# Performance work log

Measured on AMD Instinct MI355X. Metric: run time of the kernel, lower is better.

## Reference

```python
import jax, jax.numpy as jnp
import numpy as np

HIDDEN = 2048
N_HEADS = 16
HEAD_DIM = HIDDEN // N_HEADS
ROPE_THETA = 10000.0
BSZ, SEQ = 2, 2048
NEG_INF = -1e9


def setup_inputs() -> dict:
    key = jax.random.key(0)
    ks = jax.random.split(key, 5)
    scale = 1.0 / np.sqrt(HIDDEN)
    hidden_states = jax.random.normal(ks[0], (BSZ, SEQ, HIDDEN), dtype=jnp.float32)
    Wq = jax.random.normal(ks[1], (HIDDEN, HIDDEN), dtype=jnp.float32) * scale
    Wk = jax.random.normal(ks[2], (HIDDEN, HIDDEN), dtype=jnp.float32) * scale
    Wv = jax.random.normal(ks[3], (HIDDEN, HIDDEN), dtype=jnp.float32) * scale
    Wo = jax.random.normal(ks[4], (HIDDEN, HIDDEN), dtype=jnp.float32) * scale
    # additive causal mask, [1, 1, S, S]
    causal = jnp.triu(jnp.full((SEQ, SEQ), NEG_INF, dtype=jnp.float32), k=1)
    attention_mask = causal[None, None, :, :]
    position_ids = jnp.arange(SEQ, dtype=jnp.int32)
    return {
        "hidden_states": hidden_states,
        "Wq": Wq, "Wk": Wk, "Wv": Wv, "Wo": Wo,
        "attention_mask": attention_mask,
        "position_ids": position_ids,
    }


def _rotate_half(x):
    half = x.shape[-1] // 2
    return jnp.concatenate((-x[..., half:], x[..., :half]), axis=-1)


def _rope_tables(seq_len, position_ids):
    # inv_freq: [head_dim/2]
    inv_freq = 1.0 / (ROPE_THETA ** (jnp.arange(0, HEAD_DIM, 2, dtype=jnp.float32) / HEAD_DIM))
    t = jnp.arange(seq_len, dtype=jnp.float32)
    freqs = t[:, None] * inv_freq[None, :]              # [S, D/2]
    emb = jnp.concatenate((freqs, freqs), axis=-1)      # [S, D]
    cos = jnp.cos(emb)[position_ids]                    # [S, D]
    sin = jnp.sin(emb)[position_ids]
    return cos, sin


def reference(hidden_states, Wq, Wk, Wv, Wo, attention_mask, position_ids):
    b, s, h = hidden_states.shape
    def proj(W):
        return (hidden_states @ W.T).reshape(b, s, N_HEADS, HEAD_DIM).transpose(0, 2, 1, 3)
    q = proj(Wq)  # [B, H, S, D]
    k = proj(Wk)
    v = proj(Wv)
    cos, sin = _rope_tables(s, position_ids)            # [S, D], broadcasts over B,H
    q = q * cos + _rotate_half(q) * sin
    k = k * cos + _rotate_half(k) * sin
    scores = jnp.einsum('bhqd,bhkd->bhqk', q, k) / np.sqrt(HEAD_DIM)
    scores = scores + attention_mask
    w = jax.nn.softmax(scores, axis=-1)
    out = jnp.einsum('bhqk,bhkd->bhqd', w, v)           # [B, H, S, D]
    out = out.transpose(0, 2, 1, 3).reshape(b, s, h)
    return out @ Wo.T
```

## Files before the change

### kernel.cpp

```cpp
#include <hip/hip_runtime.h>
#include <cstdint>
#include <cstddef>

typedef __bf16 bf16;
typedef __bf16 bf16x4 __attribute__((ext_vector_type(4)));
typedef __bf16 bf16x8 __attribute__((ext_vector_type(8)));
typedef float  f32x4  __attribute__((ext_vector_type(4)));
typedef short  s16x4  __attribute__((ext_vector_type(4)));

#define HIDDEN 2048
#define NHEADS 16
#define HDIM   128
#define BSZ    2
#define SEQ    2048
#define BS     (BSZ*SEQ)
#define QKW    (2*HIDDEN)

union b4u { bf16x4 h; s16x4 s; };

__device__ __forceinline__ void async16(const bf16* g, bf16* l) {
    __builtin_amdgcn_global_load_lds(
        (const __attribute__((address_space(1))) unsigned int*)g,
        (__attribute__((address_space(3))) unsigned int*)l, 16, 0, 0);
}

#define BARX()  asm volatile("s_barrier" ::: "memory")
#define VMW(N)  asm volatile("s_waitcnt vmcnt(" #N ")" ::: "memory")

__device__ __forceinline__ float ex2(float x) {
    float r; asm("v_exp_f32 %0, %1" : "=v"(r) : "v"(x)); return r;
}

__global__ __launch_bounds__(256) void cast_all(const float* __restrict__ hs,
                                                const float* __restrict__ Wq,
                                                const float* __restrict__ Wk,
                                                const float* __restrict__ Wv,
                                                const float* __restrict__ Wo,
                                                const int* __restrict__ pos,
                                                bf16* __restrict__ hs_b,
                                                bf16* __restrict__ wqkv,
                                                bf16* __restrict__ wo_b,
                                                float2* __restrict__ tab) {
    int i = blockIdx.x * 256 + threadIdx.x;
    if (i >= 6291456) {
        int j = i - 6291456;
        int s = j >> 6, p = j & 63;
        float t = (float)pos[s];
        float inv = expf(-(float)(2 * p) * (9.2103403719761836f / 128.0f));
        float sn, cs;
        sincosf(t * inv, &sn, &cs);
        tab[j] = make_float2(cs, sn);
        return;
    }
    const float* src; bf16* dst; int off;
    if (i < 2097152) { src = hs; dst = hs_b; off = i; }
    else {
        int j = i - 2097152;
        int r = j >> 20;
        off = j & 1048575;
        if      (r == 0) { src = Wq; dst = wqkv; }
        else if (r == 1) { src = Wk; dst = wqkv + (size_t)4194304; }
        else if (r == 2) { src = Wv; dst = wqkv + (size_t)8388608; }
        else             { src = Wo; dst = wo_b; }
    }
    const float4 v = ((const float4*)src)[off];
    bf16x4 o;
    o.x = (bf16)v.x; o.y = (bf16)v.y; o.z = (bf16)v.z; o.w = (bf16)v.w;
    ((bf16x4*)dst)[off] = o;
}

__device__ __forceinline__ int qk_perm(int n) {
    int wl = n >> 6, j = n & 63;
    return ((wl >> 1) << 7) | ((j >> 5) << 6) | ((wl & 1) << 5) | (j & 31);
}

#define QKV_TILE(T, DOSTAGE, VMN) do {                                          \
    VMW(VMN);                                                                   \
    BARX();                                                                     \
    const bf16* lAr = lA0 + ((T) & 3) * 16384;                                  \
    const bf16* lBr = lB0 + ((T) & 3) * 16384;                                  \
    bf16x8 bfr[4], af[4];                                                       \
    _Pragma("unroll") for (int nf = 0; nf < 4; ++nf)                            \
        bfr[nf] = *(const bf16x8*)(lBr + nf * 512);                             \
    _Pragma("unroll") for (int mf = 0; mf < 4; ++mf)                            \
        af[mf] = *(const bf16x8*)(lAr + mf * 512);                              \
    if (DOSTAGE) {                                                              \
        bf16* dA = smem + (((T) + 3) & 3) * 16384 + w * 512;                    \
        async16(pa0 + ((T) + 3) * 32, dA);                                      \
        async16(pa1 + ((T) + 3) * 32, dA + 4096);                               \
    }                                                                           \
    __builtin_amdgcn_s_setprio(1);                                              \
    _Pragma("unroll") for (int mf = 0; mf < 4; ++mf)                            \
    _Pragma("unroll") for (int nf = 0; nf < 4; ++nf)                            \
        acc[mf][nf] = __builtin_amdgcn_mfma_f32_16x16x32_bf16(                  \
            af[mf], bfr[nf], acc[mf][nf], 0, 0, 0);                             \
    __builtin_amdgcn_s_setprio(0);                                              \
    _Pragma("unroll") for (int mf = 0; mf < 4; ++mf)                            \
        af[mf] = *(const bf16x8*)(lAr + 2048 + mf * 512);                       \
    if (DOSTAGE) {                                                              \
        bf16* dB = smem + (((T) + 3) & 3) * 16384 + 8192 + w * 512;             \
        async16(pb0 + ((T) + 3) * 32, dB);                                      \
        async16(pb1 + ((T) + 3) * 32, dB + 4096);                               \
    }                                                                           \
    __builtin_amdgcn_s_setprio(1);                                              \
    _Pragma("unroll") for (int mf = 0; mf < 4; ++mf)                            \
    _Pragma("unroll") for (int nf = 0; nf < 4; ++nf)                            \
        acc[4 + mf][nf] = __builtin_amdgcn_mfma_f32_16x16x32_bf16(              \
            af[mf], bfr[nf], acc[4 + mf][nf], 0, 0, 0);                         \
    __builtin_amdgcn_s_setprio(0);                                              \
} while (0)

__global__ __launch_bounds__(512, 2) void gemm_qk(const bf16* __restrict__ A,
                                                  const bf16* __restrict__ Bt,
                                                  const float2* __restrict__ tab,
                                                  bf16* __restrict__ qk) {
    __shared__ alignas(16) bf16 smem[65536];

    const int tid  = threadIdx.x;
    const int lane = tid & 63;
    const int w    = tid >> 6;
    const int l15  = lane & 15;
    const int quad = lane >> 4;
    const int wm   = w >> 2;
    const int wn   = w & 3;

    const int raw = blockIdx.x;
    const int kq  = raw >> 3;
    const int mTile = (kq & 15) * 256;
    const int nTile = (2 * (raw & 7) + (kq >> 4)) * 256;

    const int sRow  = w * 16 + (lane >> 2);
    const int sColE = ((lane & 3) * 8) ^ ((lane & 32) ? 16 : 0);
    const bf16* pa0 = A + (size_t)(mTile + sRow) * HIDDEN + sColE;
    const bf16* pa1 = pa0 + (size_t)128 * HIDDEN;
    const int n0 = qk_perm(sRow), n1 = qk_perm(sRow + 128);
    const bf16* pb0 = Bt + (size_t)(nTile + n0) * HIDDEN + sColE;
    const bf16* pb1 = Bt + (size_t)(nTile + n1) * HIDDEN + sColE;

    const int colE = (quad * 8) ^ ((l15 & 8) ? 16 : 0);
    const bf16* lA0 = smem + (wm * 128 + l15) * 32 + colE;
    const bf16* lB0 = smem + 8192 + (wn * 64 + l15) * 32 + colE;

    f32x4 acc[8][4];
#pragma unroll
    for (int i = 0; i < 8; ++i)
#pragma unroll
        for (int j = 0; j < 4; ++j) acc[i][j] = (f32x4){0.f, 0.f, 0.f, 0.f};

#pragma unroll
    for (int tt = 0; tt < 3; ++tt) {
        bf16* dA = smem + tt * 16384 + w * 512;
        async16(pa0 + tt * 32, dA);
        async16(pa1 + tt * 32, dA + 4096);
        async16(pb0 + tt * 32, dA + 8192);
        async16(pb1 + tt * 32, dA + 12288);
    }

#pragma unroll 4
    for (int t = 0; t < 60; ++t) QKV_TILE(t, 1, 8);
    QKV_TILE(60, 1, 8);
    QKV_TILE(61, 0, 8);
    QKV_TILE(62, 0, 4);
    QKV_TILE(63, 0, 0);

    const float qs = (nTile < HIDDEN) ? (0.08838834764831845f * 1.4426950408889634f) : 1.0f;
    const int hbase = nTile + (wn >> 1) * 128 + (wn & 1) * 32;
#pragma unroll
    for (int mf = 0; mf < 8; ++mf)
#pragma unroll
        for (int r = 0; r < 4; ++r) {
            int row = mTile + wm * 128 + mf * 16 + quad * 4 + r;
            int s   = row & (SEQ - 1);
            float2 t0 = tab[s * 64 + (wn & 1) * 32 + l15];
            float2 t1 = tab[s * 64 + (wn & 1) * 32 + 16 + l15];
            size_t rb = (size_t)row * QKW + hbase + l15;
            float lo0 = acc[mf][0][r], hi0 = acc[mf][2][r];
            float lo1 = acc[mf][1][r], hi1 = acc[mf][3][r];
            qk[rb]      = (bf16)((lo0 * t0.x - hi0 * t0.y) * qs);
            qk[rb + 64] = (bf16)((hi0 * t0.x + lo0 * t0.y) * qs);
            qk[rb + 16] = (bf16)((lo1 * t1.x - hi1 * t1.y) * qs);
            qk[rb + 80] = (bf16)((hi1 * t1.x + lo1 * t1.y) * qs);
        }
}

#define OUT_TILE(T, DOSTAGE, VMN) do {                                          \
    VMW(VMN);                                                                   \
    BARX();                                                                     \
    const bf16* lAr = lA0 + ((T) & 3) * 12288;                                  \
    const bf16* lBr = lB0 + ((T) & 3) * 12288;                                  \
    bf16x8 bfr[4], af[4];                                                       \
    _Pragma("unroll") for (int nf = 0; nf < 4; ++nf)                            \
        bfr[nf] = *(const bf16x8*)(lBr + nf * 512);                             \
    _Pragma("unroll") for (int mf = 0; mf < 4; ++mf)                            \
        af[mf] = *(const bf16x8*)(lAr + mf * 512);                              \
    if (DOSTAGE) {                                                              \
        bf16* dS = smem + (((T) + 3) & 3) * 12288 + w * 512;                    \
        async16(pa0 + ((T) + 3) * 32, dS);                                      \
        async16(pb0 + ((T) + 3) * 32, dS + 4096);                               \
        async16(pb1 + ((T) + 3) * 32, dS + 8192);                               \
    }                                                                           \
    __builtin_amdgcn_s_setprio(1);                                              \
    _Pragma("unroll") for (int mf = 0; mf < 4; ++mf)                            \
    _Pragma("unroll") for (int nf = 0; nf < 4; ++nf)                            \
        acc[mf][nf] = __builtin_amdgcn_mfma_f32_16x16x32_bf16(                  \
            af[mf], bfr[nf], acc[mf][nf], 0, 0, 0);                             \
    __builtin_amdgcn_s_setprio(0);                                              \
} while (0)

#define OUT_PROLOGUE()                                                          \
    const int tid  = threadIdx.x;                                               \
    const int lane = tid & 63;                                                  \
    const int w    = tid >> 6;                                                  \
    const int l15  = lane & 15;                                                 \
    const int quad = lane >> 4;                                                 \
    const int wm   = w >> 2;                                                    \
    const int wn   = w & 3;                                                     \
    const int raw = blockIdx.x;                                                 \
    const int mTile = (raw >> 3) * 128;                                         \
    const int nTile = (raw & 7) * 256;                                          \
    const int sRow  = w * 16 + (lane >> 2);                                     \
    const int sColE = ((lane & 3) * 8) ^ ((lane & 32) ? 16 : 0);                \
    const bf16* pa0 = A + (size_t)(mTile + sRow) * HIDDEN + sColE;              \
    const bf16* pb0 = Bt + (size_t)(nTile + sRow) * HIDDEN + sColE;             \
    const bf16* pb1 = pb0 + (size_t)128 * HIDDEN;                               \
    const int colE = (quad * 8) ^ ((l15 & 8) ? 16 : 0);                         \
    const bf16* lA0 = smem + (wm * 64 + l15) * 32 + colE;                       \
    const bf16* lB0 = smem + 4096 + (wn * 64 + l15) * 32 + colE;                \
    f32x4 acc[4][4];                                                            \
    _Pragma("unroll") for (int i = 0; i < 4; ++i)                               \
    _Pragma("unroll") for (int j = 0; j < 4; ++j)                               \
        acc[i][j] = (f32x4){0.f, 0.f, 0.f, 0.f};                                \
    _Pragma("unroll") for (int tt = 0; tt < 3; ++tt) {                          \
        bf16* dS = smem + tt * 12288 + w * 512;                                 \
        async16(pa0 + tt * 32, dS);                                             \
        async16(pb0 + tt * 32, dS + 4096);                                      \
        async16(pb1 + tt * 32, dS + 8192);                                      \
    }                                                                           \
    _Pragma("unroll 4") for (int t = 0; t < 60; ++t) OUT_TILE(t, 1, 6);         \
    OUT_TILE(60, 1, 6);                                                         \
    OUT_TILE(61, 0, 6);                                                         \
    OUT_TILE(62, 0, 3);                                                         \
    OUT_TILE(63, 0, 0);

__global__ __launch_bounds__(512, 2) void gemm_v(const bf16* __restrict__ A,
                                                 const bf16* __restrict__ Bt,
                                                 bf16* __restrict__ vtb) {
    __shared__ alignas(16) bf16 smem[49152];
    OUT_PROLOGUE()
#pragma unroll
    for (int mf = 0; mf < 4; ++mf)
#pragma unroll
        for (int nf = 0; nf < 4; ++nf) {
            int col_v = nTile + wn * 64 + nf * 16 + l15;
            int row0  = mTile + wm * 64 + mf * 16 + quad * 4;
            bf16x4 pk;
#pragma unroll
            for (int r = 0; r < 4; ++r) pk[r] = (bf16)acc[mf][nf][r];
            *(bf16x4*)(vtb + (size_t)col_v * BS + row0) = pk;
        }
}

__global__ __launch_bounds__(512, 2) void gemm_out(const bf16* __restrict__ A,
                                                   const bf16* __restrict__ Bt,
                                                   float* __restrict__ C) {
    __shared__ alignas(16) bf16 smem[49152];
    OUT_PROLOGUE()
#pragma unroll
    for (int mf = 0; mf < 4; ++mf)
#pragma unroll
        for (int nf = 0; nf < 4; ++nf)
#pragma unroll
            for (int r = 0; r < 4; ++r) {
                int row = mTile + wm * 64 + mf * 16 + quad * 4 + r;
                int col = nTile + wn * 64 + nf * 16 + l15;
                C[(size_t)row * HIDDEN + col] = acc[mf][nf][r];
            }
}

__global__ __launch_bounds__(256, 2) void attn_kernel(const bf16* __restrict__ qk,
                                                      const bf16* __restrict__ vt,
                                                      bf16* __restrict__ ao) {
    __shared__ bf16 Kls[2][64 * 128];
    __shared__ bf16 Vls[2][128 * 64];

    const int tid  = threadIdx.x;
    const int lane = tid & 63;
    const int w    = tid >> 6;
    const int l15  = lane & 15;
    const int quad = lane >> 4;
    const int bid  = blockIdx.x;
    const int half = bid >> 8;
    const int idx  = bid & 255;
    const int qb2  = half ? (idx >> 5) : 15 - (idx >> 5);
    const int bh   = idx & 31;
    const int b    = bh >> 4;
    const int h    = bh & 15;
    const int qbase = qb2 * 128;
    const int nt    = 2 * qb2 + 2;
    const size_t seq0 = (size_t)b * SEQ;

    bf16x8 qf[2][4];
#pragma unroll
    for (int qs = 0; qs < 2; ++qs) {
        const bf16* qp = qk + (seq0 + qbase + w * 32 + qs * 16 + l15) * QKW + h * HDIM + quad * 8;
#pragma unroll
        for (int ks = 0; ks < 4; ++ks) qf[qs][ks] = *(const bf16x8*)(qp + ks * 32);
    }
#pragma unroll
    for (int qs = 0; qs < 2; ++qs)
#pragma unroll
        for (int ks = 0; ks < 4; ++ks)
            asm volatile("" :: "v"(*(const f32x4*)&qf[qs][ks]));

    f32x4 o[8][2];
#pragma unroll
    for (int i = 0; i < 8; ++i)
#pragma unroll
        for (int qs = 0; qs < 2; ++qs) o[i][qs] = (f32x4){0.f, 0.f, 0.f, 0.f};
    float m_s[2] = {-3e38f, -3e38f}, l_s[2] = {0.f, 0.f};
    int qg[2];
#pragma unroll
    for (int qs = 0; qs < 2; ++qs) qg[qs] = qbase + w * 32 + qs * 16 + l15;

    const int krow = lane >> 4;
    const int kp   = lane & 15;
    const int vrow = lane >> 3;
    const int vp   = lane & 7;
    const int sw   = l15 & 7;

    const bf16* qksrc = qk + seq0 * QKW + HIDDEN + h * HDIM;
    const bf16* vtsrc = vt + (size_t)h * HDIM * BS + seq0;
    int koff[4], voff[4];
#pragma unroll
    for (int i = 0; i < 4; ++i) {
        int c = w * 4 + i;
        int j = c * 4 + krow;
        int c2 = (kp & 8) | ((kp & 7) ^ (j & 7));
        koff[i] = j * QKW + c2 * 8;
        int d = c * 8 + vrow;
        int cv = vp ^ (d & 7);
        voff[i] = d * BS + cv * 8;
    }

    const bf16* kbase[4];
#pragma unroll
    for (int ks = 0; ks < 4; ++ks)
        kbase[ks] = &Kls[0][l15 * 128 + (((ks * 4 + quad) ^ sw) << 3)];
    const bf16* vbase[4];
#pragma unroll
    for (int ni = 0; ni < 4; ++ni)
        vbase[ni] = &Vls[0][l15 * 64 + ((((ni * 2 + (quad >> 1)) ^ sw) << 3) + (quad & 1) * 4)];

#define ATTN_STAGE(T, BUF) do {                                                  \
        const int kb_ = (T) * 64;                                                \
        _Pragma("unroll") for (int i = 0; i < 4; ++i)                            \
            async16(qksrc + (size_t)kb_ * QKW + koff[i],                         \
                    &Kls[BUF][(w * 4 + i) * 512]);                               \
        _Pragma("unroll") for (int i = 0; i < 4; ++i)                            \
            async16(vtsrc + kb_ + voff[i],                                       \
                    &Vls[BUF][(w * 4 + i) * 512]);                               \
    } while (0)

#define ATTN_TILE(T, BUF) do {                                                   \
        if ((T) + 1 < nt) { ATTN_STAGE((T) + 1, (BUF) ^ 1); VMW(8); }            \
        else              { VMW(0); }                                            \
        BARX();                                                                  \
        const int kb = (T) * 64;                                                 \
        f32x4 sa[4][2];                                                          \
        _Pragma("unroll") for (int ni = 0; ni < 4; ++ni)                         \
        _Pragma("unroll") for (int qs = 0; qs < 2; ++qs)                         \
            sa[ni][qs] = (f32x4){0.f, 0.f, 0.f, 0.f};                            \
        _Pragma("unroll") for (int ni = 0; ni < 4; ++ni)                         \
        _Pragma("unroll") for (int ks = 0; ks < 4; ++ks) {                       \
            bf16x8 kf = *(const bf16x8*)(kbase[ks] + (BUF) * 8192 + ni * 2048);  \
            sa[ni][0] = __builtin_amdgcn_mfma_f32_16x16x32_bf16(kf, qf[0][ks], sa[ni][0], 0, 0, 0); \
            sa[ni][1] = __builtin_amdgcn_mfma_f32_16x16x32_bf16(kf, qf[1][ks], sa[ni][1], 0, 0, 0); \
        }                                                                        \
        const bool diag = ((T) >= nt - 2);                                       \
        b4u pb[4][2];                                                            \
        _Pragma("unroll") for (int qs = 0; qs < 2; ++qs) {                       \
            float rmax = -3e38f;                                                 \
            _Pragma("unroll") for (int ni = 0; ni < 4; ++ni)                     \
            _Pragma("unroll") for (int r = 0; r < 4; ++r) {                      \
                float sv = sa[ni][qs][r];                                        \
                if (diag && (kb + ni * 16 + quad * 4 + r > qg[qs])) sv = -1e30f; \
                sa[ni][qs][r] = sv;                                              \
                rmax = fmaxf(rmax, sv);                                          \
            }                                                                    \
            rmax = fmaxf(rmax, __shfl_xor(rmax, 16));                            \
            rmax = fmaxf(rmax, __shfl_xor(rmax, 32));                            \
            if (__ballot(rmax > m_s[qs] + 8.f) != 0ull) {                        \
                float mn = fmaxf(m_s[qs], rmax);                                 \
                float al = ex2(m_s[qs] - mn);                                    \
                m_s[qs] = mn; l_s[qs] *= al;                                     \
                _Pragma("unroll") for (int n2 = 0; n2 < 8; ++n2)                 \
                _Pragma("unroll") for (int r = 0; r < 4; ++r) o[n2][qs][r] *= al;\
            }                                                                    \
            float rsum = 0.f;                                                    \
            _Pragma("unroll") for (int ni = 0; ni < 4; ++ni)                     \
            _Pragma("unroll") for (int r = 0; r < 4; ++r) {                      \
                float e = ex2(sa[ni][qs][r] - m_s[qs]);                          \
                rsum += e;                                                       \
                pb[ni][qs].h[r] = (bf16)e;                                       \
            }                                                                    \
            rsum += __shfl_xor(rsum, 16);                                        \
            rsum += __shfl_xor(rsum, 32);                                        \
            l_s[qs] += rsum;                                                     \
        }                                                                        \
        _Pragma("unroll") for (int n2 = 0; n2 < 8; ++n2)                         \
        _Pragma("unroll") for (int ni = 0; ni < 4; ++ni) {                       \
            b4u vf;                                                              \
            vf.h = *(const bf16x4*)(vbase[ni] + (BUF) * 8192 + n2 * 1024);       \
            o[n2][0] = __builtin_amdgcn_mfma_f32_16x16x16bf16_1k(vf.s, pb[ni][0].s, o[n2][0], 0, 0, 0); \
            o[n2][1] = __builtin_amdgcn_mfma_f32_16x16x16bf16_1k(vf.s, pb[ni][1].s, o[n2][1], 0, 0, 0); \
        }                                                                        \
        BARX();                                                                  \
    } while (0)

    ATTN_STAGE(0, 0);
    for (int t = 0; t < nt; t += 2) {
        ATTN_TILE(t, 0);
        ATTN_TILE(t + 1, 1);
    }
#undef ATTN_TILE
#undef ATTN_STAGE

#pragma unroll
    for (int qs = 0; qs < 2; ++qs) {
        const float inv = 1.0f / l_s[qs];
        bf16* op = ao + (seq0 + qg[qs]) * HIDDEN + h * HDIM + quad * 4;
#pragma unroll
        for (int n2 = 0; n2 < 8; ++n2) {
            bf16x4 pk;
#pragma unroll
            for (int r = 0; r < 4; ++r) pk[r] = (bf16)(o[n2][qs][r] * inv);
            *(bf16x4*)(op + n2 * 16) = pk;
        }
    }
}

extern "C" void kernel_launch(void* const* d_in, const int* in_sizes, int n_in,
                              void* d_out, int out_size, void* d_ws, size_t ws_size,
                              hipStream_t stream) {
    const float* hs = (const float*)d_in[0];
    const float* Wq = (const float*)d_in[1];
    const float* Wk = (const float*)d_in[2];
    const float* Wv = (const float*)d_in[3];
    const float* Wo = (const float*)d_in[4];
    const int* pos  = (const int*)d_in[6];
    float* out = (float*)d_out;

    bf16* hs_b = (bf16*)d_ws;
    bf16* wqkv = hs_b + (size_t)8388608;
    bf16* wo_b = wqkv + (size_t)12582912;
    bf16* qkb  = wo_b + (size_t)4194304;
    bf16* vtb  = qkb + (size_t)16777216;
    bf16* ao   = vtb + (size_t)8388608;
    float2* tab = (float2*)ao;

    cast_all<<<25088, 256, 0, stream>>>(hs, Wq, Wk, Wv, Wo, pos, hs_b, wqkv, wo_b, tab);
    gemm_qk<<<256, 512, 0, stream>>>(hs_b, wqkv, tab, qkb);
    gemm_v<<<256, 512, 0, stream>>>(hs_b, wqkv + (size_t)8388608, vtb);
    attn_kernel<<<512, 256, 0, stream>>>(qkb, vtb, ao);
    gemm_out<<<256, 512, 0, stream>>>(ao, wo_b, out);
}
```

Measured before the change: 372.5 us.

## Single-buffer attention K/V tiles with split K/V prefetch and higher occupancy

```diff
diff --git a/kernel.cpp b/kernel.cpp
--- a/kernel.cpp
+++ b/kernel.cpp
@@ -277,11 +277,11 @@
             }
 }
 
-__global__ __launch_bounds__(256, 2) void attn_kernel(const bf16* __restrict__ qk,
+__global__ __launch_bounds__(256, 4) void attn_kernel(const bf16* __restrict__ qk,
                                                       const bf16* __restrict__ vt,
                                                       bf16* __restrict__ ao) {
-    __shared__ bf16 Kls[2][64 * 128];
-    __shared__ bf16 Vls[2][128 * 64];
+    __shared__ bf16 Kls[64 * 128];
+    __shared__ bf16 Vls[128 * 64];
 
     const int tid  = threadIdx.x;
     const int lane = tid & 63;
@@ -289,10 +289,8 @@
     const int l15  = lane & 15;
     const int quad = lane >> 4;
     const int bid  = blockIdx.x;
-    const int half = bid >> 8;
-    const int idx  = bid & 255;
-    const int qb2  = half ? (idx >> 5) : 15 - (idx >> 5);
-    const int bh   = idx & 31;
+    const int qb2  = 15 - (bid >> 5);
+    const int bh   = bid & 31;
     const int b    = bh >> 4;
     const int h    = bh & 15;
     const int qbase = qb2 * 128;
@@ -345,85 +343,108 @@
     const bf16* kbase[4];
 #pragma unroll
     for (int ks = 0; ks < 4; ++ks)
-        kbase[ks] = &Kls[0][l15 * 128 + (((ks * 4 + quad) ^ sw) << 3)];
+        kbase[ks] = &Kls[l15 * 128 + (((ks * 4 + quad) ^ sw) << 3)];
     const bf16* vbase[4];
 #pragma unroll
     for (int ni = 0; ni < 4; ++ni)
-        vbase[ni] = &Vls[0][l15 * 64 + ((((ni * 2 + (quad >> 1)) ^ sw) << 3) + (quad & 1) * 4)];
-
-#define ATTN_STAGE(T, BUF) do {                                                  \
-        const int kb_ = (T) * 64;                                                \
+        vbase[ni] = &Vls[l15 * 64 + ((((ni * 2 + (quad >> 1)) ^ sw) << 3) + (quad & 1) * 4)];
+
+#define STAGE_K(T) do {                                                          \
         _Pragma("unroll") for (int i = 0; i < 4; ++i)                            \
-            async16(qksrc + (size_t)kb_ * QKW + koff[i],                         \
-                    &Kls[BUF][(w * 4 + i) * 512]);                               \
+            async16(qksrc + (size_t)((T) * 64) * QKW + koff[i],                  \
+                    &Kls[(w * 4 + i) * 512]);                                    \
+    } while (0)
+#define STAGE_V(T) do {                                                          \
         _Pragma("unroll") for (int i = 0; i < 4; ++i)                            \
-            async16(vtsrc + kb_ + voff[i],                                       \
-                    &Vls[BUF][(w * 4 + i) * 512]);                               \
+            async16(vtsrc + (T) * 64 + voff[i],                                  \
+                    &Vls[(w * 4 + i) * 512]);                                    \
     } while (0)
 
-#define ATTN_TILE(T, BUF) do {                                                   \
-        if ((T) + 1 < nt) { ATTN_STAGE((T) + 1, (BUF) ^ 1); VMW(8); }            \
-        else              { VMW(0); }                                            \
-        BARX();                                                                  \
-        const int kb = (T) * 64;                                                 \
-        f32x4 sa[4][2];                                                          \
-        _Pragma("unroll") for (int ni = 0; ni < 4; ++ni)                         \
-        _Pragma("unroll") for (int qs = 0; qs < 2; ++qs)                         \
-            sa[ni][qs] = (f32x4){0.f, 0.f, 0.f, 0.f};                            \
-        _Pragma("unroll") for (int ni = 0; ni < 4; ++ni)                         \
-        _Pragma("unroll") for (int ks = 0; ks < 4; ++ks) {                       \
-            bf16x8 kf = *(const bf16x8*)(kbase[ks] + (BUF) * 8192 + ni * 2048);  \
-            sa[ni][0] = __builtin_amdgcn_mfma_f32_16x16x32_bf16(kf, qf[0][ks], sa[ni][0], 0, 0, 0); \
-            sa[ni][1] = __builtin_amdgcn_mfma_f32_16x16x32_bf16(kf, qf[1][ks], sa[ni][1], 0, 0, 0); \
-        }                                                                        \
-        const bool diag = ((T) >= nt - 2);                                       \
-        b4u pb[4][2];                                                            \
-        _Pragma("unroll") for (int qs = 0; qs < 2; ++qs) {                       \
-            float rmax = -3e38f;                                                 \
-            _Pragma("unroll") for (int ni = 0; ni < 4; ++ni)                     \
-            _Pragma("unroll") for (int r = 0; r < 4; ++r) {                      \
-                float sv = sa[ni][qs][r];                                        \
-                if (diag && (kb + ni * 16 + quad * 4 + r > qg[qs])) sv = -1e30f; \
-                sa[ni][qs][r] = sv;                                              \
-                rmax = fmaxf(rmax, sv);                                          \
-            }                                                                    \
-            rmax = fmaxf(rmax, __shfl_xor(rmax, 16));                            \
-            rmax = fmaxf(rmax, __shfl_xor(rmax, 32));                            \
-            if (__ballot(rmax > m_s[qs] + 8.f) != 0ull) {                        \
-                float mn = fmaxf(m_s[qs], rmax);                                 \
-                float al = ex2(m_s[qs] - mn);                                    \
-                m_s[qs] = mn; l_s[qs] *= al;                                     \
-                _Pragma("unroll") for (int n2 = 0; n2 < 8; ++n2)                 \
-                _Pragma("unroll") for (int r = 0; r < 4; ++r) o[n2][qs][r] *= al;\
-            }                                                                    \
-            float rsum = 0.f;                                                    \
-            _Pragma("unroll") for (int ni = 0; ni < 4; ++ni)                     \
-            _Pragma("unroll") for (int r = 0; r < 4; ++r) {                      \
-                float e = ex2(sa[ni][qs][r] - m_s[qs]);                          \
-                rsum += e;                                                       \
-                pb[ni][qs].h[r] = (bf16)e;                                       \
-            }                                                                    \
-            rsum += __shfl_xor(rsum, 16);                                        \
-            rsum += __shfl_xor(rsum, 32);                                        \
-            l_s[qs] += rsum;                                                     \
-        }                                                                        \
-        _Pragma("unroll") for (int n2 = 0; n2 < 8; ++n2)                         \
-        _Pragma("unroll") for (int ni = 0; ni < 4; ++ni) {                       \
-            b4u vf;                                                              \
-            vf.h = *(const bf16x4*)(vbase[ni] + (BUF) * 8192 + n2 * 1024);       \
-            o[n2][0] = __builtin_amdgcn_mfma_f32_16x16x16bf16_1k(vf.s, pb[ni][0].s, o[n2][0], 0, 0, 0); \
-            o[n2][1] = __builtin_amdgcn_mfma_f32_16x16x16bf16_1k(vf.s, pb[ni][1].s, o[n2][1], 0, 0, 0); \
-        }                                                                        \
-        BARX();                                                                  \
-    } while (0)
-
-    ATTN_STAGE(0, 0);
-    for (int t = 0; t < nt; t += 2) {
-        ATTN_TILE(t, 0);
-        ATTN_TILE(t + 1, 1);
-    }
-#undef ATTN_TILE
-#undef ATTN_STAGE
+    STAGE_K(0);
+    STAGE_V(0);
+
+    for (int t = 0; t < nt; ++t) {
+        VMW(4);
+        BARX();
+        const int kb = t * 64;
+
+        f32x4 sa[4][2];
+#pragma unroll
+        for (int ni = 0; ni < 4; ++ni)
+#pragma unroll
+            for (int qs = 0; qs < 2; ++qs) sa[ni][qs] = (f32x4){0.f, 0.f, 0.f, 0.f};
+        __builtin_amdgcn_s_setprio(1);
+#pragma unroll
+        for (int ni = 0; ni < 4; ++ni)
+#pragma unroll
+            for (int ks = 0; ks < 4; ++ks) {
+                bf16x8 kf = *(const bf16x8*)(kbase[ks] + ni * 2048);
+                sa[ni][0] = __builtin_amdgcn_mfma_f32_16x16x32_bf16(kf, qf[0][ks], sa[ni][0], 0, 0, 0);
+                sa[ni][1] = __builtin_amdgcn_mfma_f32_16x16x32_bf16(kf, qf[1][ks], sa[ni][1], 0, 0, 0);
+            }
+        __builtin_amdgcn_s_setprio(0);
+        BARX();
+        if (t + 1 < nt) STAGE_K(t + 1);
+
+        const bool diag = (t >= nt - 2);
+        b4u pb[4][2];
+#pragma unroll
+        for (int qs = 0; qs < 2; ++qs) {
+            float rmax = -3e38f;
+#pragma unroll
+            for (int ni = 0; ni < 4; ++ni)
+#pragma unroll
+                for (int r = 0; r < 4; ++r) {
+                    float sv = sa[ni][qs][r];
+                    if (diag && (kb + ni * 16 + quad * 4 + r > qg[qs])) sv = -1e30f;
+                    sa[ni][qs][r] = sv;
+                    rmax = fmaxf(rmax, sv);
+                }
+            rmax = fmaxf(rmax, __shfl_xor(rmax, 16));
+            rmax = fmaxf(rmax, __shfl_xor(rmax, 32));
+            if (__ballot(rmax > m_s[qs] + 8.f) != 0ull) {
+                float mn = fmaxf(m_s[qs], rmax);
+                float al = ex2(m_s[qs] - mn);
+                m_s[qs] = mn; l_s[qs] *= al;
+#pragma unroll
+                for (int n2 = 0; n2 < 8; ++n2)
+#pragma unroll
+                    for (int r = 0; r < 4; ++r) o[n2][qs][r] *= al;
+            }
+            float rsum = 0.f;
+#pragma unroll
+            for (int ni = 0; ni < 4; ++ni)
+#pragma unroll
+                for (int r = 0; r < 4; ++r) {
+                    float e = ex2(sa[ni][qs][r] - m_s[qs]);
+                    rsum += e;
+                    pb[ni][qs].h[r] = (bf16)e;
+                }
+            rsum += __shfl_xor(rsum, 16);
+            rsum += __shfl_xor(rsum, 32);
+            l_s[qs] += rsum;
+        }
+
+        if (t + 1 < nt) { VMW(4); }
+        else            { VMW(0); }
+        BARX();
+
+        __builtin_amdgcn_s_setprio(1);
+#pragma unroll
+        for (int n2 = 0; n2 < 8; ++n2)
+#pragma unroll
+            for (int ni = 0; ni < 4; ++ni) {
+                b4u vf;
+                vf.h = *(const bf16x4*)(vbase[ni] + n2 * 1024);
+                o[n2][0] = __builtin_amdgcn_mfma_f32_16x16x16bf16_1k(vf.s, pb[ni][0].s, o[n2][0], 0, 0, 0);
+                o[n2][1] = __builtin_amdgcn_mfma_f32_16x16x16bf16_1k(vf.s, pb[ni][1].s, o[n2][1], 0, 0, 0);
+            }
+        __builtin_amdgcn_s_setprio(0);
+        BARX();
+        if (t + 1 < nt) STAGE_V(t + 1);
+    }
+#undef STAGE_K
+#undef STAGE_V
 
 #pragma unroll
     for (int qs = 0; qs < 2; ++qs) {
```

Result: slower. 517.6 us (+39.0%).
